# Kernel tuning notes

Hardware: AMD Instinct MI355X
Metric: run time of the kernel (lower is better)

Reference implementation:

```python
import jax, jax.numpy as jnp
import numpy as np

NUM_ITERATIONS = 3
EPS = 1e-7

def squash(v, axis=-1):
    # scale = |v|^2/(1+|v|^2) * v/sqrt(|v|^2+eps), matching the torch module
    sq = jnp.sum(v * v, axis=axis, keepdims=True)
    return (sq / (1.0 + sq)) * v / jnp.sqrt(sq + EPS)

def setup_inputs() -> dict:
    key = jax.random.key(0)
    kx, kw = jax.random.split(key)
    B, R, C, O, I = 256, 1152, 10, 16, 8
    x = jax.random.normal(kx, (B, R, I), dtype=jnp.float32)
    W = jax.random.normal(kw, (R, C, O, I), dtype=jnp.float32)
    return {"x": x, "W": W}

def reference(x, W):
    B, R, I = x.shape
    C, O = W.shape[1], W.shape[2]
    # u_hat[b,r,c,o] = sum_i W[r,c,o,i] * x[b,r,i]  (batched tiny GEMV)
    u_hat = jnp.einsum('rcoi,bri->brco', W, x)
    b_ij = jnp.zeros((B, R, C), dtype=u_hat.dtype)
    v = None
    for it in range(NUM_ITERATIONS):
        c_ij = jax.nn.softmax(b_ij, axis=1)          # softmax over route nodes (dim=1, as in source)
        s_j = jnp.einsum('brc,brco->bco', c_ij, u_hat)
        v = squash(s_j, axis=-1)                      # squash over out_channels (dim=-2 of the 5D torch tensor)
        if it != NUM_ITERATIONS - 1:
            b_ij = b_ij + jnp.einsum('brco,bco->brc', u_hat, v)
    # match torch output shape (B, 1, C, O, 1)
    return v[:, None, :, :, None]
```

## Files before the change

kernel.cpp:

```cpp
#include <hip/hip_runtime.h>
#include <cstdint>

#define BB 256
#define RR 1152
#define CC 10
#define OO 16
#define II 8
#define NT 768
#define GG 2
#define NWAVE (NT / 64)
#define LOG2E 1.4426950408889634f

typedef float float2v __attribute__((ext_vector_type(2)));

__device__ __forceinline__ float bflo(uint32_t pk) {
    union { uint32_t i; float f; } a; a.i = pk << 16; return a.f;
}
__device__ __forceinline__ float bfhi(uint32_t pk) {
    union { uint32_t i; float f; } a; a.i = pk & 0xffff0000u; return a.f;
}
__device__ __forceinline__ float dot4pk(float4 a, float4 b) {
    float2v al = { a.x, a.y }, ah = { a.z, a.w };
    float2v bl = { b.x, b.y }, bh = { b.z, b.w };
    float2v h = __builtin_elementwise_fma(ah, bh, al * bl);
    return h.x + h.y;
}
__device__ __forceinline__ float qpadd1(float v) {
    int o = __builtin_amdgcn_mov_dpp(__float_as_int(v), 0xB1, 0xF, 0xF, true);
    return v + __int_as_float(o);
}
__device__ __forceinline__ float qpadd2(float v) {
    int o = __builtin_amdgcn_mov_dpp(__float_as_int(v), 0x4E, 0xF, 0xF, true);
    return v + __int_as_float(o);
}
__device__ __forceinline__ float dppx2f(float v) {
    return __int_as_float(__builtin_amdgcn_mov_dpp(__float_as_int(v), 0x4E, 0xF, 0xF, true));
}
__device__ __forceinline__ uint32_t cvtpk(float lo, float hi) {
    uint32_t r;
    asm("v_cvt_pk_bf16_f32 %0, %1, %2" : "=v"(r) : "v"(lo), "v"(hi));
    return r;
}
#if __has_builtin(__builtin_amdgcn_exp2f)
#define EXP2(x) __builtin_amdgcn_exp2f(x)
#else
#define EXP2(x) __expf((x) * 0.6931471805599453f)
#endif

__global__ __launch_bounds__(NT, 6)
void k_caps(const float* __restrict__ x, const float* __restrict__ W,
            float* __restrict__ out) {
    extern __shared__ uint32_t u2[];
    __shared__ float part[NWAVE][17];
    __shared__ float p0s[NWAVE][8][4][GG];
    __shared__ float wsum[GG][OO];

    const int t = threadIdx.x;
    const int c  = blockIdx.x / (BB / GG);
    const int b0 = (blockIdx.x % (BB / GG)) * GG;
    const int wv = t >> 6, l = t & 63;
    const int rg = t >> 3, p = t & 7;

    uint32_t* uA = u2;
    uint32_t* uB = u2 + (size_t)RR * 8;

    const int pos = (p >> 1) + ((p & 1) << 2);
    uint32_t* wrA = uA + (size_t)rg * 8 + pos;
    uint32_t* wrB = uB + (size_t)rg * 8 + pos;
    const bool pb0 = (p & 1) != 0, pb1 = (p & 2) != 0;

    float s00 = 0.f, s01 = 0.f, s02 = 0.f, s03 = 0.f;
    float s10 = 0.f, s11 = 0.f, s12 = 0.f, s13 = 0.f;
    const float* wbase = W + ((size_t)rg * CC + c) * (OO * II) + p * 4;
    const float* xbase = x + ((size_t)b0 * RR + rg) * II + (p & 1) * 4;
    const size_t WSTEP = (size_t)96 * CC * OO * II;
    const size_t XSTEP = (size_t)96 * II;
    float4 cw0 = *reinterpret_cast<const float4*>(wbase);
    float4 cw1 = *reinterpret_cast<const float4*>(wbase + 32);
    float4 cw2 = *reinterpret_cast<const float4*>(wbase + 64);
    float4 cw3 = *reinterpret_cast<const float4*>(wbase + 96);
    float4 cx0 = *reinterpret_cast<const float4*>(xbase);
    float4 cx1 = *reinterpret_cast<const float4*>(xbase + (size_t)RR * II);
#pragma unroll
    for (int it = 0; it < 12; ++it) {
        float4 w0 = cw0, w1 = cw1, w2 = cw2, w3 = cw3;
        float4 xh0 = cx0, xh1 = cx1;
        if (it < 11) {
            const float* nw = wbase + (size_t)(it + 1) * WSTEP;
            cw0 = *reinterpret_cast<const float4*>(nw);
            cw1 = *reinterpret_cast<const float4*>(nw + 32);
            cw2 = *reinterpret_cast<const float4*>(nw + 64);
            cw3 = *reinterpret_cast<const float4*>(nw + 96);
            const float* nx = xbase + (size_t)(it + 1) * XSTEP;
            cx0 = *reinterpret_cast<const float4*>(nx);
            cx1 = *reinterpret_cast<const float4*>(nx + (size_t)RR * II);
        }
        {
            float d0 = qpadd1(dot4pk(w0, xh0));
            float d1 = qpadd1(dot4pk(w1, xh0));
            float d2 = qpadd1(dot4pk(w2, xh0));
            float d3 = qpadd1(dot4pk(w3, xh0));
            s00 += d0; s01 += d1; s02 += d2; s03 += d3;
            float sa = pb1 ? (pb0 ? d3 : d2) : (pb0 ? d1 : d0);
            float sb = pb1 ? (pb0 ? d1 : d0) : (pb0 ? d3 : d2);
            wrA[(size_t)it * 768] = cvtpk(sa, dppx2f(sb));
        }
        {
            float e0 = qpadd1(dot4pk(w0, xh1));
            float e1 = qpadd1(dot4pk(w1, xh1));
            float e2 = qpadd1(dot4pk(w2, xh1));
            float e3 = qpadd1(dot4pk(w3, xh1));
            s10 += e0; s11 += e1; s12 += e2; s13 += e3;
            float sa = pb1 ? (pb0 ? e3 : e2) : (pb0 ? e1 : e0);
            float sb = pb1 ? (pb0 ? e1 : e0) : (pb0 ? e3 : e2);
            wrB[(size_t)it * 768] = cvtpk(sa, dppx2f(sb));
        }
    }
#pragma unroll
    for (int m = 8; m < 64; m <<= 1) {
        s00 += __shfl_xor(s00, m); s01 += __shfl_xor(s01, m);
        s02 += __shfl_xor(s02, m); s03 += __shfl_xor(s03, m);
        s10 += __shfl_xor(s10, m); s11 += __shfl_xor(s11, m);
        s12 += __shfl_xor(s12, m); s13 += __shfl_xor(s13, m);
    }
    if (l < 8) {
        p0s[wv][l][0][0] = s00; p0s[wv][l][1][0] = s01;
        p0s[wv][l][2][0] = s02; p0s[wv][l][3][0] = s03;
        p0s[wv][l][0][1] = s10; p0s[wv][l][1][1] = s11;
        p0s[wv][l][2][1] = s12; p0s[wv][l][3][1] = s13;
    }
    __syncthreads();

    const int g2 = wv / 6;
    const int wv6 = wv - g2 * 6;
    const uint32_t* ug = g2 ? uB : uA;
    const int q = l & 3;
    const int rl = l >> 2;
    const int rbase = wv6 * 16 + rl;
    const uint32_t* rp = ug + (size_t)rbase * 8 + 2 * q;

    uint2 pv[12];
#pragma unroll
    for (int it2 = 0; it2 < 12; ++it2)
        pv[it2] = *reinterpret_cast<const uint2*>(rp + (size_t)it2 * 768);

    if (t < GG * OO) {
        const int g = t >> 4, o = t & 15;
        float s = 0.f;
#pragma unroll
        for (int w = 0; w < NWAVE; ++w) s += p0s[w][2 * (o & 3)][o >> 2][g];
        s *= (1.0f / RR);
        float ss = s * s;
        ss += __shfl_xor(ss, 1); ss += __shfl_xor(ss, 2);
        ss += __shfl_xor(ss, 4); ss += __shfl_xor(ss, 8);
        wsum[g][o] = s * (ss / ((1.0f + ss) * sqrtf(ss + 1e-7f)));
    }
    __syncthreads();

    for (int pass = 1; pass < 3; ++pass) {
        const float2v WQA = { wsum[g2][2 * q] * LOG2E,
                              wsum[g2][2 * q + 8] * LOG2E };
        const float2v WQB = { wsum[g2][2 * q + 1] * LOG2E,
                              wsum[g2][2 * q + 9] * LOG2E };
        float2v N0 = { 0.f, 0.f }, N1 = { 0.f, 0.f };
        float den = 0.f;

#pragma unroll
        for (int it2 = 0; it2 < 12; ++it2) {
            uint2 pp = pv[it2];
            float2v P0 = { bflo(pp.x), bfhi(pp.y) };
            float2v P1 = { bfhi(pp.x), bflo(pp.y) };
            float2v lg2 = __builtin_elementwise_fma(P0, WQA, P1 * WQB);
            float lg = lg2.x + lg2.y;
            lg = qpadd1(lg);
            lg = qpadd2(lg);
            float e = EXP2(lg);
            den += e;
            float2v E2 = { e, e };
            N0 = __builtin_elementwise_fma(E2, P0, N0);
            N1 = __builtin_elementwise_fma(E2, P1, N1);
        }

        float n0 = N0.x, n2 = N0.y, n1 = N1.x, n3 = N1.y;
#pragma unroll
        for (int m = 4; m < 64; m <<= 1) {
            n0 += __shfl_xor(n0, m); n1 += __shfl_xor(n1, m);
            n2 += __shfl_xor(n2, m); n3 += __shfl_xor(n3, m);
            den += __shfl_xor(den, m);
        }
        if (l < 4) {
            part[wv][2 * l]     = n0;
            part[wv][2 * l + 1] = n1;
            part[wv][2 * l + 8] = n2;
            part[wv][2 * l + 9] = n3;
            if (l == 0) part[wv][16] = den;
        }
        __syncthreads();

        if (t < GG * OO) {
            const int g = t >> 4, o = t & 15;
            float nf = 0.f, df = 0.f;
#pragma unroll
            for (int w = 0; w < 6; ++w) {
                nf += part[6 * g + w][o];
                df += part[6 * g + w][16];
            }
            float s = nf / df;
            float ss = s * s;
            ss += __shfl_xor(ss, 1); ss += __shfl_xor(ss, 2);
            ss += __shfl_xor(ss, 4); ss += __shfl_xor(ss, 8);
            float v = s * (ss / ((1.0f + ss) * sqrtf(ss + 1e-7f)));
            if (pass == 2)
                out[((size_t)(b0 + g) * CC + c) * OO + o] = v;
            else
                wsum[g][o] += v;
        }
        __syncthreads();
    }
}

extern "C" void kernel_launch(void* const* d_in, const int* in_sizes, int n_in,
                              void* d_out, int out_size, void* d_ws, size_t ws_size,
                              hipStream_t stream) {
    const float* x = (const float*)d_in[0];
    const float* W = (const float*)d_in[1];
    if (n_in >= 2 && in_sizes[0] == RR * CC * OO * II &&
        in_sizes[1] == BB * RR * II) {
        const float* tmp = x; x = W; W = tmp;
    }
    float* out = (float*)d_out;

    const size_t dyn_lds = (size_t)GG * RR * 8 * 4;
    k_caps<<<CC * (BB / GG), NT, dyn_lds, stream>>>(x, W, out);
}
```

Baseline: 105.7 us.

## Keep u_hat in registers per thread instead of staging through LDS

The thread-to-route mapping changes so each quad of lanes computes the u_hat values for its own 16 routes (8 W float4 loads per iteration, 6 iterations). The packed bf16 results stay in registers for the routing passes instead of being written to and re-read from dynamic LDS. This removes the dynamic shared allocation, the LDS write/read traffic, and the software prefetch. Each wave now handles both batch elements in the routing loop. The cost is higher register pressure, loss of the explicit prefetch pipelining, and twice as many W lanes computing per-lane dot products that are then discarded by a select.

```diff
diff --git a/kernel.cpp b/kernel.cpp
--- a/kernel.cpp
+++ b/kernel.cpp
@@ -13,11 +13,10 @@
 
 typedef float float2v __attribute__((ext_vector_type(2)));
 
-__device__ __forceinline__ float bflo(uint32_t pk) {
-    union { uint32_t i; float f; } a; a.i = pk << 16; return a.f;
-}
-__device__ __forceinline__ float bfhi(uint32_t pk) {
-    union { uint32_t i; float f; } a; a.i = pk & 0xffff0000u; return a.f;
+__device__ __forceinline__ void unpack2(uint32_t pk, float& lo, float& hi) {
+    union { uint32_t i; float f; } a, b;
+    a.i = pk << 16; b.i = pk & 0xffff0000u;
+    lo = a.f; hi = b.f;
 }
 __device__ __forceinline__ float dot4pk(float4 a, float4 b) {
     float2v al = { a.x, a.y }, ah = { a.z, a.w };
@@ -33,9 +32,6 @@
     int o = __builtin_amdgcn_mov_dpp(__float_as_int(v), 0x4E, 0xF, 0xF, true);
     return v + __int_as_float(o);
 }
-__device__ __forceinline__ float dppx2f(float v) {
-    return __int_as_float(__builtin_amdgcn_mov_dpp(__float_as_int(v), 0x4E, 0xF, 0xF, true));
-}
 __device__ __forceinline__ uint32_t cvtpk(float lo, float hi) {
     uint32_t r;
     asm("v_cvt_pk_bf16_f32 %0, %1, %2" : "=v"(r) : "v"(lo), "v"(hi));
@@ -50,80 +46,79 @@
 __global__ __launch_bounds__(NT, 6)
 void k_caps(const float* __restrict__ x, const float* __restrict__ W,
             float* __restrict__ out) {
-    extern __shared__ uint32_t u2[];
-    __shared__ float part[NWAVE][17];
-    __shared__ float p0s[NWAVE][8][4][GG];
+    __shared__ float part[NWAVE][GG][18];
+    __shared__ float p0s[NWAVE][4][4][GG];
     __shared__ float wsum[GG][OO];
 
     const int t = threadIdx.x;
     const int c  = blockIdx.x / (BB / GG);
     const int b0 = (blockIdx.x % (BB / GG)) * GG;
     const int wv = t >> 6, l = t & 63;
-    const int rg = t >> 3, p = t & 7;
-
-    uint32_t* uA = u2;
-    uint32_t* uB = u2 + (size_t)RR * 8;
-
-    const int pos = (p >> 1) + ((p & 1) << 2);
-    uint32_t* wrA = uA + (size_t)rg * 8 + pos;
-    uint32_t* wrB = uB + (size_t)rg * 8 + pos;
-    const bool pb0 = (p & 1) != 0, pb1 = (p & 2) != 0;
-
+    const int q = l & 3, rl = l >> 2;
+    const int r0 = wv * 16 + rl;
+    const int off = 2 * (q & 1) + (q >> 1);
+    const bool qb = (q & 1) != 0;
+
+    uint32_t st[6][GG][2];
     float s00 = 0.f, s01 = 0.f, s02 = 0.f, s03 = 0.f;
     float s10 = 0.f, s11 = 0.f, s12 = 0.f, s13 = 0.f;
-    const float* wbase = W + ((size_t)rg * CC + c) * (OO * II) + p * 4;
-    const float* xbase = x + ((size_t)b0 * RR + rg) * II + (p & 1) * 4;
-    const size_t WSTEP = (size_t)96 * CC * OO * II;
-    const size_t XSTEP = (size_t)96 * II;
-    float4 cw0 = *reinterpret_cast<const float4*>(wbase);
-    float4 cw1 = *reinterpret_cast<const float4*>(wbase + 32);
-    float4 cw2 = *reinterpret_cast<const float4*>(wbase + 64);
-    float4 cw3 = *reinterpret_cast<const float4*>(wbase + 96);
-    float4 cx0 = *reinterpret_cast<const float4*>(xbase);
-    float4 cx1 = *reinterpret_cast<const float4*>(xbase + (size_t)RR * II);
-#pragma unroll
-    for (int it = 0; it < 12; ++it) {
-        float4 w0 = cw0, w1 = cw1, w2 = cw2, w3 = cw3;
-        float4 xh0 = cx0, xh1 = cx1;
-        if (it < 11) {
-            const float* nw = wbase + (size_t)(it + 1) * WSTEP;
-            cw0 = *reinterpret_cast<const float4*>(nw);
-            cw1 = *reinterpret_cast<const float4*>(nw + 32);
-            cw2 = *reinterpret_cast<const float4*>(nw + 64);
-            cw3 = *reinterpret_cast<const float4*>(nw + 96);
-            const float* nx = xbase + (size_t)(it + 1) * XSTEP;
-            cx0 = *reinterpret_cast<const float4*>(nx);
-            cx1 = *reinterpret_cast<const float4*>(nx + (size_t)RR * II);
-        }
+
+    const float* wb  = W + ((size_t)r0 * CC + c) * (OO * II) + 4 * q;
+    const float* xb0 = x + ((size_t)b0 * RR + r0) * II + 4 * (q & 1);
+    const float* xb1 = xb0 + (size_t)RR * II;
+
+#pragma unroll
+    for (int it = 0; it < 6; ++it) {
+        const float* wp = wb + (size_t)it * (192 * CC * OO * II);
+        float4 w0 = *reinterpret_cast<const float4*>(wp);
+        float4 w1 = *reinterpret_cast<const float4*>(wp + 16);
+        float4 w2 = *reinterpret_cast<const float4*>(wp + 32);
+        float4 w3 = *reinterpret_cast<const float4*>(wp + 48);
+        float4 w4 = *reinterpret_cast<const float4*>(wp + 64);
+        float4 w5 = *reinterpret_cast<const float4*>(wp + 80);
+        float4 w6 = *reinterpret_cast<const float4*>(wp + 96);
+        float4 w7 = *reinterpret_cast<const float4*>(wp + 112);
+        float4 xa = *reinterpret_cast<const float4*>(xb0 + (size_t)it * 192 * II);
+        float4 xc = *reinterpret_cast<const float4*>(xb1 + (size_t)it * 192 * II);
         {
-            float d0 = qpadd1(dot4pk(w0, xh0));
-            float d1 = qpadd1(dot4pk(w1, xh0));
-            float d2 = qpadd1(dot4pk(w2, xh0));
-            float d3 = qpadd1(dot4pk(w3, xh0));
+            float f0 = qpadd1(dot4pk(w0, xa));
+            float f1 = qpadd1(dot4pk(w1, xa));
+            float f2 = qpadd1(dot4pk(w2, xa));
+            float f3 = qpadd1(dot4pk(w3, xa));
+            float f4 = qpadd1(dot4pk(w4, xa));
+            float f5 = qpadd1(dot4pk(w5, xa));
+            float f6 = qpadd1(dot4pk(w6, xa));
+            float f7 = qpadd1(dot4pk(w7, xa));
+            float d0 = qb ? f1 : f0, d1 = qb ? f3 : f2;
+            float d2 = qb ? f5 : f4, d3 = qb ? f7 : f6;
             s00 += d0; s01 += d1; s02 += d2; s03 += d3;
-            float sa = pb1 ? (pb0 ? d3 : d2) : (pb0 ? d1 : d0);
-            float sb = pb1 ? (pb0 ? d1 : d0) : (pb0 ? d3 : d2);
-            wrA[(size_t)it * 768] = cvtpk(sa, dppx2f(sb));
+            st[it][0][0] = cvtpk(d0, d1);
+            st[it][0][1] = cvtpk(d2, d3);
         }
         {
-            float e0 = qpadd1(dot4pk(w0, xh1));
-            float e1 = qpadd1(dot4pk(w1, xh1));
-            float e2 = qpadd1(dot4pk(w2, xh1));
-            float e3 = qpadd1(dot4pk(w3, xh1));
-            s10 += e0; s11 += e1; s12 += e2; s13 += e3;
-            float sa = pb1 ? (pb0 ? e3 : e2) : (pb0 ? e1 : e0);
-            float sb = pb1 ? (pb0 ? e1 : e0) : (pb0 ? e3 : e2);
-            wrB[(size_t)it * 768] = cvtpk(sa, dppx2f(sb));
-        }
-    }
-#pragma unroll
-    for (int m = 8; m < 64; m <<= 1) {
+            float f0 = qpadd1(dot4pk(w0, xc));
+            float f1 = qpadd1(dot4pk(w1, xc));
+            float f2 = qpadd1(dot4pk(w2, xc));
+            float f3 = qpadd1(dot4pk(w3, xc));
+            float f4 = qpadd1(dot4pk(w4, xc));
+            float f5 = qpadd1(dot4pk(w5, xc));
+            float f6 = qpadd1(dot4pk(w6, xc));
+            float f7 = qpadd1(dot4pk(w7, xc));
+            float d0 = qb ? f1 : f0, d1 = qb ? f3 : f2;
+            float d2 = qb ? f5 : f4, d3 = qb ? f7 : f6;
+            s10 += d0; s11 += d1; s12 += d2; s13 += d3;
+            st[it][1][0] = cvtpk(d0, d1);
+            st[it][1][1] = cvtpk(d2, d3);
+        }
+    }
+#pragma unroll
+    for (int m = 4; m < 64; m <<= 1) {
         s00 += __shfl_xor(s00, m); s01 += __shfl_xor(s01, m);
         s02 += __shfl_xor(s02, m); s03 += __shfl_xor(s03, m);
         s10 += __shfl_xor(s10, m); s11 += __shfl_xor(s11, m);
         s12 += __shfl_xor(s12, m); s13 += __shfl_xor(s13, m);
     }
-    if (l < 8) {
+    if (l < 4) {
         p0s[wv][l][0][0] = s00; p0s[wv][l][1][0] = s01;
         p0s[wv][l][2][0] = s02; p0s[wv][l][3][0] = s03;
         p0s[wv][l][0][1] = s10; p0s[wv][l][1][1] = s11;
@@ -131,24 +126,14 @@
     }
     __syncthreads();
 
-    const int g2 = wv / 6;
-    const int wv6 = wv - g2 * 6;
-    const uint32_t* ug = g2 ? uB : uA;
-    const int q = l & 3;
-    const int rl = l >> 2;
-    const int rbase = wv6 * 16 + rl;
-    const uint32_t* rp = ug + (size_t)rbase * 8 + 2 * q;
-
-    uint2 pv[12];
-#pragma unroll
-    for (int it2 = 0; it2 < 12; ++it2)
-        pv[it2] = *reinterpret_cast<const uint2*>(rp + (size_t)it2 * 768);
-
     if (t < GG * OO) {
         const int g = t >> 4, o = t & 15;
+        const int rem = o & 3;
+        const int qo = (rem >> 1) + 2 * (rem & 1);
+        const int jo = o >> 2;
         float s = 0.f;
 #pragma unroll
-        for (int w = 0; w < NWAVE; ++w) s += p0s[w][2 * (o & 3)][o >> 2][g];
+        for (int w = 0; w < NWAVE; ++w) s += p0s[w][qo][jo][g];
         s *= (1.0f / RR);
         float ss = s * s;
         ss += __shfl_xor(ss, 1); ss += __shfl_xor(ss, 2);
@@ -157,43 +142,64 @@
     }
     __syncthreads();
 
+#pragma unroll
     for (int pass = 1; pass < 3; ++pass) {
-        const float2v WQA = { wsum[g2][2 * q] * LOG2E,
-                              wsum[g2][2 * q + 8] * LOG2E };
-        const float2v WQB = { wsum[g2][2 * q + 1] * LOG2E,
-                              wsum[g2][2 * q + 9] * LOG2E };
-        float2v N0 = { 0.f, 0.f }, N1 = { 0.f, 0.f };
-        float den = 0.f;
-
-#pragma unroll
-        for (int it2 = 0; it2 < 12; ++it2) {
-            uint2 pp = pv[it2];
-            float2v P0 = { bflo(pp.x), bfhi(pp.y) };
-            float2v P1 = { bfhi(pp.x), bflo(pp.y) };
-            float2v lg2 = __builtin_elementwise_fma(P0, WQA, P1 * WQB);
-            float lg = lg2.x + lg2.y;
-            lg = qpadd1(lg);
-            lg = qpadd2(lg);
-            float e = EXP2(lg);
-            den += e;
-            float2v E2 = { e, e };
-            N0 = __builtin_elementwise_fma(E2, P0, N0);
-            N1 = __builtin_elementwise_fma(E2, P1, N1);
-        }
-
-        float n0 = N0.x, n2 = N0.y, n1 = N1.x, n3 = N1.y;
+        float wq00 = wsum[0][off]      * LOG2E, wq01 = wsum[0][4 + off] * LOG2E;
+        float wq02 = wsum[0][8 + off]  * LOG2E, wq03 = wsum[0][12 + off] * LOG2E;
+        float wq10 = wsum[1][off]      * LOG2E, wq11 = wsum[1][4 + off] * LOG2E;
+        float wq12 = wsum[1][8 + off]  * LOG2E, wq13 = wsum[1][12 + off] * LOG2E;
+        float n00 = 0.f, n01 = 0.f, n02 = 0.f, n03 = 0.f;
+        float n10 = 0.f, n11 = 0.f, n12 = 0.f, n13 = 0.f;
+        float den0 = 0.f, den1 = 0.f;
+
+#pragma unroll
+        for (int it = 0; it < 6; ++it) {
+            {
+                float u0, u1, u2, u3;
+                unpack2(st[it][0][0], u0, u1);
+                unpack2(st[it][0][1], u2, u3);
+                float lg = u0 * wq00;
+                lg = fmaf(u1, wq01, lg);
+                lg = fmaf(u2, wq02, lg);
+                lg = fmaf(u3, wq03, lg);
+                lg = qpadd1(lg);
+                lg = qpadd2(lg);
+                float e = EXP2(lg);
+                den0 += e;
+                n00 = fmaf(e, u0, n00); n01 = fmaf(e, u1, n01);
+                n02 = fmaf(e, u2, n02); n03 = fmaf(e, u3, n03);
+            }
+            {
+                float u0, u1, u2, u3;
+                unpack2(st[it][1][0], u0, u1);
+                unpack2(st[it][1][1], u2, u3);
+                float lg = u0 * wq10;
+                lg = fmaf(u1, wq11, lg);
+                lg = fmaf(u2, wq12, lg);
+                lg = fmaf(u3, wq13, lg);
+                lg = qpadd1(lg);
+                lg = qpadd2(lg);
+                float e = EXP2(lg);
+                den1 += e;
+                n10 = fmaf(e, u0, n10); n11 = fmaf(e, u1, n11);
+                n12 = fmaf(e, u2, n12); n13 = fmaf(e, u3, n13);
+            }
+        }
+
 #pragma unroll
         for (int m = 4; m < 64; m <<= 1) {
-            n0 += __shfl_xor(n0, m); n1 += __shfl_xor(n1, m);
-            n2 += __shfl_xor(n2, m); n3 += __shfl_xor(n3, m);
-            den += __shfl_xor(den, m);
+            n00 += __shfl_xor(n00, m); n01 += __shfl_xor(n01, m);
+            n02 += __shfl_xor(n02, m); n03 += __shfl_xor(n03, m);
+            n10 += __shfl_xor(n10, m); n11 += __shfl_xor(n11, m);
+            n12 += __shfl_xor(n12, m); n13 += __shfl_xor(n13, m);
+            den0 += __shfl_xor(den0, m); den1 += __shfl_xor(den1, m);
         }
         if (l < 4) {
-            part[wv][2 * l]     = n0;
-            part[wv][2 * l + 1] = n1;
-            part[wv][2 * l + 8] = n2;
-            part[wv][2 * l + 9] = n3;
-            if (l == 0) part[wv][16] = den;
+            part[wv][0][off]      = n00; part[wv][0][4 + off]  = n01;
+            part[wv][0][8 + off]  = n02; part[wv][0][12 + off] = n03;
+            part[wv][1][off]      = n10; part[wv][1][4 + off]  = n11;
+            part[wv][1][8 + off]  = n12; part[wv][1][12 + off] = n13;
+            if (l == 0) { part[wv][0][16] = den0; part[wv][1][16] = den1; }
         }
         __syncthreads();
 
@@ -201,9 +207,9 @@
             const int g = t >> 4, o = t & 15;
             float nf = 0.f, df = 0.f;
 #pragma unroll
-            for (int w = 0; w < 6; ++w) {
-                nf += part[6 * g + w][o];
-                df += part[6 * g + w][16];
+            for (int w = 0; w < NWAVE; ++w) {
+                nf += part[w][g][o];
+                df += part[w][g][16];
             }
             float s = nf / df;
             float ss = s * s;
@@ -230,6 +236,5 @@
     }
     float* out = (float*)d_out;
 
-    const size_t dyn_lds = (size_t)GG * RR * 8 * 4;
-    k_caps<<<CC * (BB / GG), NT, dyn_lds, stream>>>(x, W, out);
-}
+    k_caps<<<CC * (BB / GG), NT, 0, stream>>>(x, W, out);
+}
```

Result: slower. 123.5 us (+16.8%).

## Process four batch elements per block to reuse W loads across more batches

Applied to the files above, without the earlier changes.

Raises the batch group per block from 2 to 4, so each W row load is reused for four x vectors, halving global W traffic and the number of blocks. The routing pass now reads packed u_hat from LDS every iteration instead of caching it in registers, and the software prefetch of the next W/x tile is dropped in favour of a partially unrolled loop. Dynamic LDS doubles, which cuts occupancy (launch bounds lowered to 3) and needs an opt-in attribute for the larger shared allocation.

```diff
diff --git a/kernel.cpp b/kernel.cpp
--- a/kernel.cpp
+++ b/kernel.cpp
@@ -7,17 +7,17 @@
 #define OO 16
 #define II 8
 #define NT 768
-#define GG 2
+#define GG 4
 #define NWAVE (NT / 64)
+#define WPG (NWAVE / GG)
 #define LOG2E 1.4426950408889634f
 
 typedef float float2v __attribute__((ext_vector_type(2)));
 
-__device__ __forceinline__ float bflo(uint32_t pk) {
-    union { uint32_t i; float f; } a; a.i = pk << 16; return a.f;
-}
-__device__ __forceinline__ float bfhi(uint32_t pk) {
-    union { uint32_t i; float f; } a; a.i = pk & 0xffff0000u; return a.f;
+__device__ __forceinline__ void unpack2(uint32_t pk, float& lo, float& hi) {
+    union { uint32_t i; float f; } a, b;
+    a.i = pk << 16; b.i = pk & 0xffff0000u;
+    lo = a.f; hi = b.f;
 }
 __device__ __forceinline__ float dot4pk(float4 a, float4 b) {
     float2v al = { a.x, a.y }, ah = { a.z, a.w };
@@ -46,8 +46,21 @@
 #else
 #define EXP2(x) __expf((x) * 0.6931471805599453f)
 #endif
-
-__global__ __launch_bounds__(NT, 6)
+#define LD4(P) (*reinterpret_cast<const float4*>(P))
+
+#define P1G(XV, SG0, SG1, SG2, SG3, WR)                                       \
+  do {                                                                        \
+    float d0 = qpadd1(dot4pk(w0, XV));                                        \
+    float d1 = qpadd1(dot4pk(w1, XV));                                        \
+    float d2 = qpadd1(dot4pk(w2, XV));                                        \
+    float d3 = qpadd1(dot4pk(w3, XV));                                        \
+    SG0 += d0; SG1 += d1; SG2 += d2; SG3 += d3;                               \
+    float sa = pb1 ? (pb0 ? d3 : d2) : (pb0 ? d1 : d0);                       \
+    float sb = pb1 ? (pb0 ? d1 : d0) : (pb0 ? d3 : d2);                       \
+    (WR)[(size_t)it * 768] = cvtpk(sa, dppx2f(sb));                           \
+  } while (0)
+
+__global__ __launch_bounds__(NT, 3)
 void k_caps(const float* __restrict__ x, const float* __restrict__ W,
             float* __restrict__ out) {
     extern __shared__ uint32_t u2[];
@@ -63,58 +76,37 @@
 
     uint32_t* uA = u2;
     uint32_t* uB = u2 + (size_t)RR * 8;
+    uint32_t* uC = u2 + (size_t)2 * RR * 8;
+    uint32_t* uD = u2 + (size_t)3 * RR * 8;
 
     const int pos = (p >> 1) + ((p & 1) << 2);
     uint32_t* wrA = uA + (size_t)rg * 8 + pos;
     uint32_t* wrB = uB + (size_t)rg * 8 + pos;
+    uint32_t* wrC = uC + (size_t)rg * 8 + pos;
+    uint32_t* wrD = uD + (size_t)rg * 8 + pos;
     const bool pb0 = (p & 1) != 0, pb1 = (p & 2) != 0;
 
     float s00 = 0.f, s01 = 0.f, s02 = 0.f, s03 = 0.f;
     float s10 = 0.f, s11 = 0.f, s12 = 0.f, s13 = 0.f;
-    const float* wbase = W + ((size_t)rg * CC + c) * (OO * II) + p * 4;
-    const float* xbase = x + ((size_t)b0 * RR + rg) * II + (p & 1) * 4;
-    const size_t WSTEP = (size_t)96 * CC * OO * II;
-    const size_t XSTEP = (size_t)96 * II;
-    float4 cw0 = *reinterpret_cast<const float4*>(wbase);
-    float4 cw1 = *reinterpret_cast<const float4*>(wbase + 32);
-    float4 cw2 = *reinterpret_cast<const float4*>(wbase + 64);
-    float4 cw3 = *reinterpret_cast<const float4*>(wbase + 96);
-    float4 cx0 = *reinterpret_cast<const float4*>(xbase);
-    float4 cx1 = *reinterpret_cast<const float4*>(xbase + (size_t)RR * II);
-#pragma unroll
+    float s20 = 0.f, s21 = 0.f, s22 = 0.f, s23 = 0.f;
+    float s30 = 0.f, s31 = 0.f, s32 = 0.f, s33 = 0.f;
+#pragma unroll 2
     for (int it = 0; it < 12; ++it) {
-        float4 w0 = cw0, w1 = cw1, w2 = cw2, w3 = cw3;
-        float4 xh0 = cx0, xh1 = cx1;
-        if (it < 11) {
-            const float* nw = wbase + (size_t)(it + 1) * WSTEP;
-            cw0 = *reinterpret_cast<const float4*>(nw);
-            cw1 = *reinterpret_cast<const float4*>(nw + 32);
-            cw2 = *reinterpret_cast<const float4*>(nw + 64);
-            cw3 = *reinterpret_cast<const float4*>(nw + 96);
-            const float* nx = xbase + (size_t)(it + 1) * XSTEP;
-            cx0 = *reinterpret_cast<const float4*>(nx);
-            cx1 = *reinterpret_cast<const float4*>(nx + (size_t)RR * II);
-        }
-        {
-            float d0 = qpadd1(dot4pk(w0, xh0));
-            float d1 = qpadd1(dot4pk(w1, xh0));
-            float d2 = qpadd1(dot4pk(w2, xh0));
-            float d3 = qpadd1(dot4pk(w3, xh0));
-            s00 += d0; s01 += d1; s02 += d2; s03 += d3;
-            float sa = pb1 ? (pb0 ? d3 : d2) : (pb0 ? d1 : d0);
-            float sb = pb1 ? (pb0 ? d1 : d0) : (pb0 ? d3 : d2);
-            wrA[(size_t)it * 768] = cvtpk(sa, dppx2f(sb));
-        }
-        {
-            float e0 = qpadd1(dot4pk(w0, xh1));
-            float e1 = qpadd1(dot4pk(w1, xh1));
-            float e2 = qpadd1(dot4pk(w2, xh1));
-            float e3 = qpadd1(dot4pk(w3, xh1));
-            s10 += e0; s11 += e1; s12 += e2; s13 += e3;
-            float sa = pb1 ? (pb0 ? e3 : e2) : (pb0 ? e1 : e0);
-            float sb = pb1 ? (pb0 ? e1 : e0) : (pb0 ? e3 : e2);
-            wrB[(size_t)it * 768] = cvtpk(sa, dppx2f(sb));
-        }
+        const int r = it * 96 + rg;
+        const float* wrow = W + ((size_t)r * CC + c) * (OO * II) + p * 4;
+        float4 w0 = LD4(wrow);
+        float4 w1 = LD4(wrow + 32);
+        float4 w2 = LD4(wrow + 64);
+        float4 w3 = LD4(wrow + 96);
+        const float* xp = x + ((size_t)b0 * RR + r) * II + (p & 1) * 4;
+        float4 xa = LD4(xp);
+        float4 xb = LD4(xp + (size_t)RR * II);
+        float4 xc = LD4(xp + (size_t)2 * RR * II);
+        float4 xd = LD4(xp + (size_t)3 * RR * II);
+        P1G(xa, s00, s01, s02, s03, wrA);
+        P1G(xb, s10, s11, s12, s13, wrB);
+        P1G(xc, s20, s21, s22, s23, wrC);
+        P1G(xd, s30, s31, s32, s33, wrD);
     }
 #pragma unroll
     for (int m = 8; m < 64; m <<= 1) {
@@ -122,27 +114,22 @@
         s02 += __shfl_xor(s02, m); s03 += __shfl_xor(s03, m);
         s10 += __shfl_xor(s10, m); s11 += __shfl_xor(s11, m);
         s12 += __shfl_xor(s12, m); s13 += __shfl_xor(s13, m);
+        s20 += __shfl_xor(s20, m); s21 += __shfl_xor(s21, m);
+        s22 += __shfl_xor(s22, m); s23 += __shfl_xor(s23, m);
+        s30 += __shfl_xor(s30, m); s31 += __shfl_xor(s31, m);
+        s32 += __shfl_xor(s32, m); s33 += __shfl_xor(s33, m);
     }
     if (l < 8) {
         p0s[wv][l][0][0] = s00; p0s[wv][l][1][0] = s01;
         p0s[wv][l][2][0] = s02; p0s[wv][l][3][0] = s03;
         p0s[wv][l][0][1] = s10; p0s[wv][l][1][1] = s11;
         p0s[wv][l][2][1] = s12; p0s[wv][l][3][1] = s13;
+        p0s[wv][l][0][2] = s20; p0s[wv][l][1][2] = s21;
+        p0s[wv][l][2][2] = s22; p0s[wv][l][3][2] = s23;
+        p0s[wv][l][0][3] = s30; p0s[wv][l][1][3] = s31;
+        p0s[wv][l][2][3] = s32; p0s[wv][l][3][3] = s33;
     }
     __syncthreads();
-
-    const int g2 = wv / 6;
-    const int wv6 = wv - g2 * 6;
-    const uint32_t* ug = g2 ? uB : uA;
-    const int q = l & 3;
-    const int rl = l >> 2;
-    const int rbase = wv6 * 16 + rl;
-    const uint32_t* rp = ug + (size_t)rbase * 8 + 2 * q;
-
-    uint2 pv[12];
-#pragma unroll
-    for (int it2 = 0; it2 < 12; ++it2)
-        pv[it2] = *reinterpret_cast<const uint2*>(rp + (size_t)it2 * 768);
 
     if (t < GG * OO) {
         const int g = t >> 4, o = t & 15;
@@ -156,6 +143,14 @@
         wsum[g][o] = s * (ss / ((1.0f + ss) * sqrtf(ss + 1e-7f)));
     }
     __syncthreads();
+
+    const int g2 = wv / WPG;
+    const int wv3 = wv - g2 * WPG;
+    const uint32_t* ug = u2 + (size_t)g2 * RR * 8;
+    const int q = l & 3;
+    const int rl = l >> 2;
+    const int rbase = wv3 * 16 + rl;
+    const uint32_t* rp = ug + (size_t)rbase * 8 + 2 * q;
 
     for (int pass = 1; pass < 3; ++pass) {
         const float2v WQA = { wsum[g2][2 * q] * LOG2E,
@@ -166,10 +161,16 @@
         float den = 0.f;
 
 #pragma unroll
-        for (int it2 = 0; it2 < 12; ++it2) {
-            uint2 pp = pv[it2];
-            float2v P0 = { bflo(pp.x), bfhi(pp.y) };
-            float2v P1 = { bfhi(pp.x), bflo(pp.y) };
+        for (int it2 = 0; it2 < 24; ++it2) {
+            uint2 pp = *reinterpret_cast<const uint2*>(rp + (size_t)it2 * 384);
+            float2v P0, P1;
+            {
+                float u0, u1, u2f, u3;
+                unpack2(pp.x, u0, u1);
+                unpack2(pp.y, u3, u2f);
+                P0.x = u0; P0.y = u2f;
+                P1.x = u1; P1.y = u3;
+            }
             float2v lg2 = __builtin_elementwise_fma(P0, WQA, P1 * WQB);
             float lg = lg2.x + lg2.y;
             lg = qpadd1(lg);
@@ -201,9 +202,9 @@
             const int g = t >> 4, o = t & 15;
             float nf = 0.f, df = 0.f;
 #pragma unroll
-            for (int w = 0; w < 6; ++w) {
-                nf += part[6 * g + w][o];
-                df += part[6 * g + w][16];
+            for (int w = 0; w < WPG; ++w) {
+                nf += part[WPG * g + w][o];
+                df += part[WPG * g + w][16];
             }
             float s = nf / df;
             float ss = s * s;
@@ -231,5 +232,12 @@
     float* out = (float*)d_out;
 
     const size_t dyn_lds = (size_t)GG * RR * 8 * 4;
+    static bool s_attr = false;
+    if (!s_attr) {
+        hipFuncSetAttribute(reinterpret_cast<const void*>(k_caps),
+                            hipFuncAttributeMaxDynamicSharedMemorySize,
+                            (int)dyn_lds);
+        s_attr = true;
+    }
     k_caps<<<CC * (BB / GG), NT, dyn_lds, stream>>>(x, W, out);
 }
```

New measurement: 114.2 us. +8.0%, slower.
